# Kernel tuning notes

Measured on AMD Instinct MI355X. Metric: run time of the kernel, lower is better.

The kernel has to match this reference:

```python
import jax, jax.numpy as jnp
import numpy as np

EMBED_DIM = 1024
NUM_HEADS = 16
HEAD_DIM = EMBED_DIM // NUM_HEADS
BATCH = 2
SEQ = 2048


def setup_inputs() -> dict:
    key = jax.random.key(0)
    ks = jax.random.split(key, 10)
    s = 1.0 / np.sqrt(EMBED_DIM)
    inp = {
        "query": jax.random.normal(ks[0], (BATCH, SEQ, EMBED_DIM), jnp.float32),
        # Linear weights stored as [in, out] (y = x @ W + b)
        "wq": jax.random.normal(ks[1], (EMBED_DIM, EMBED_DIM), jnp.float32) * s,
        "bq": jnp.zeros((EMBED_DIM,), jnp.float32),
        "wk": jax.random.normal(ks[2], (EMBED_DIM, EMBED_DIM), jnp.float32) * s,
        "bk": jnp.zeros((EMBED_DIM,), jnp.float32),
        "wv": jax.random.normal(ks[3], (EMBED_DIM, EMBED_DIM), jnp.float32) * s,
        "bv": jnp.zeros((EMBED_DIM,), jnp.float32),
        "wo": jax.random.normal(ks[4], (EMBED_DIM, EMBED_DIM), jnp.float32) * s,
        "bo": jnp.zeros((EMBED_DIM,), jnp.float32),
        "temperature": jnp.float32(HEAD_DIM),  # learnable temperature, init = head_dim
    }
    return inp


def reference(query, wq, bq, wk, bk, wv, bv, wo, bo, temperature):
    B, S, E = query.shape
    # self-attention: key = value = query
    Q = (query @ wq + bq).reshape(B, S, NUM_HEADS, HEAD_DIM).transpose(0, 2, 1, 3)
    K = (query @ wk + bk).reshape(B, S, NUM_HEADS, HEAD_DIM).transpose(0, 2, 1, 3)
    V = (query @ wv + bv).reshape(B, S, NUM_HEADS, HEAD_DIM).transpose(0, 2, 1, 3)
    # squared Euclidean distances: ||q||^2 + ||k||^2 - 2<q,k>
    q_sq = jnp.sum(Q * Q, axis=-1, keepdims=True)          # (B,H,Sq,1)
    k_sq = jnp.sum(K * K, axis=-1, keepdims=True)          # (B,H,Sk,1)
    qk = jnp.einsum("bhqd,bhkd->bhqk", Q, K)
    d_sq = jnp.maximum(q_sq + jnp.swapaxes(k_sq, -2, -1) - 2.0 * qk, 0.0)
    attn = jax.nn.softmax(-d_sq / temperature, axis=-1)    # (B,H,Sq,Sk)
    out = jnp.einsum("bhqk,bhkd->bhqd", attn, V)
    out = out.transpose(0, 2, 1, 3).reshape(B, S, E)
    return out @ wo + bo
```

## Files before the change

### kernel.cpp

```cpp
#include <hip/hip_runtime.h>
#include <stdint.h>
#include <stddef.h>


#define LOG2E 1.44269504088896f

typedef __attribute__((ext_vector_type(8))) short bf16x8;
typedef __attribute__((ext_vector_type(4))) float f32x4;
typedef __attribute__((ext_vector_type(4))) unsigned short u16x4;

__device__ __forceinline__ unsigned short f2b(float f) {
  union { float f; unsigned int u; } x; x.f = f;
  unsigned int u = x.u;
  u += 0x7fffu + ((u >> 16) & 1u);
  return (unsigned short)(u >> 16);
}
__device__ __forceinline__ float b2f(unsigned short s) {
  union { unsigned int u; float f; } x; x.u = ((unsigned int)s) << 16;
  return x.f;
}
__device__ __forceinline__ unsigned int fbits(float f) {
  union { float f; unsigned int u; } x; x.f = f; return x.u;
}

#define GLD_LDS(g, l) __builtin_amdgcn_global_load_lds( \
    (const __attribute__((address_space(1))) void*)(g), \
    (__attribute__((address_space(3))) void*)(l), 16, 0, 0)

__global__ void prep_kernel(const float* __restrict__ X,
                            const float* __restrict__ wq, const float* __restrict__ wk,
                            const float* __restrict__ wv, const float* __restrict__ wo,
                            unsigned short* __restrict__ Xb,
                            unsigned short* __restrict__ WTqkv, unsigned short* __restrict__ WTo) {
  int z = blockIdx.z;
  if (z == 4) {
    size_t base = ((size_t)(blockIdx.y * 16 + blockIdx.x)) * 16384;
    #pragma unroll
    for (int j = 0; j < 16; ++j) {
      size_t i = base + (size_t)(j * 256 + threadIdx.x) * 4;
      f32x4 v = *(const f32x4*)&X[i];
      u16x4 o;
      #pragma unroll
      for (int k = 0; k < 4; ++k) o[k] = f2b(v[k]);
      *(u16x4*)&Xb[i] = o;
    }
    return;
  }
  __shared__ float tile[64][65];
  const float* src = (z == 0) ? wq : (z == 1) ? wk : (z == 2) ? wv : wo;
  unsigned short* dst = (z < 3) ? (WTqkv + (size_t)z * 1024 * 1024) : WTo;
  int k0 = blockIdx.y * 64, n0 = blockIdx.x * 64;
  int rr = threadIdx.x >> 6, cc = threadIdx.x & 63;
  #pragma unroll
  for (int p = 0; p < 16; ++p) {
    int row = p * 4 + rr;
    tile[row][cc] = src[(size_t)(k0 + row) * 1024 + n0 + cc];
  }
  __syncthreads();
  #pragma unroll
  for (int p = 0; p < 16; ++p) {
    int row = p * 4 + rr;
    dst[(size_t)(n0 + row) * 1024 + k0 + cc] = f2b(tile[cc][row]);
  }
}

__global__ __launch_bounds__(256, 3) void gemm_qkv_kernel(
    const unsigned short* __restrict__ X, const unsigned short* __restrict__ WT,
    const float* __restrict__ bq, const float* __restrict__ bk, const float* __restrict__ bv,
    const float* __restrict__ temp,
    unsigned short* __restrict__ Qb, unsigned short* __restrict__ Kb,
    unsigned short* __restrict__ VTo, float* __restrict__ ks2) {
  __shared__ __align__(16) unsigned short smem[16896];
  unsigned short* As = smem;
  unsigned short* Bs = smem + 8192;
  const int t = threadIdx.x, w = t >> 6, lane = t & 63;
  const int r = lane & 15, q4 = lane >> 4;
  const int m0 = blockIdx.y * 128, n0 = blockIdx.x * 128;
  const int wr = (w >> 1) * 64, wc = (w & 1) * 64;
  const unsigned short* Xg = X + (size_t)m0 * 1024;
  const unsigned short* Wg = WT + (size_t)n0 * 1024;
  f32x4 acc[4][4] = {};
  for (int k0 = 0; k0 < 1024; k0 += 64) {
    #pragma unroll
    for (int g = 0; g < 4; ++g) {
      int slot = g * 256 + t;
      int kh = slot >> 9, row = (slot >> 2) & 127, ko = (slot & 3) * 8;
      GLD_LDS(Xg + (size_t)row * 1024 + k0 + kh * 32 + ko, &As[(g * 256 + w * 64) * 8]);
      GLD_LDS(Wg + (size_t)row * 1024 + k0 + kh * 32 + ko, &Bs[(g * 256 + w * 64) * 8]);
    }
    __syncthreads();
    #pragma unroll
    for (int kh = 0; kh < 2; ++kh) {
      bf16x8 af[4], bfr[4];
      #pragma unroll
      for (int mf = 0; mf < 4; ++mf)
        af[mf] = *(const bf16x8*)&As[kh * 4096 + (wr + mf * 16 + r) * 32 + q4 * 8];
      #pragma unroll
      for (int nf = 0; nf < 4; ++nf)
        bfr[nf] = *(const bf16x8*)&Bs[kh * 4096 + (wc + nf * 16 + r) * 32 + q4 * 8];
      #pragma unroll
      for (int mf = 0; mf < 4; ++mf)
        #pragma unroll
        for (int nf = 0; nf < 4; ++nf)
          acc[mf][nf] = __builtin_amdgcn_mfma_f32_16x16x32_bf16(af[mf], bfr[nf], acc[mf][nf], 0, 0, 0);
    }
    __syncthreads();
  }
  const int nblk = n0 >> 10;
  if (nblk == 0) {
    const int nc0 = n0 & 1023;
    #pragma unroll
    for (int nf = 0; nf < 4; ++nf) {
      int n = nc0 + wc + nf * 16 + r;
      float bb = bq[n];
      #pragma unroll
      for (int mf = 0; mf < 4; ++mf) {
        int m = m0 + wr + mf * 16 + q4 * 4;
        f32x4 v = acc[mf][nf];
        #pragma unroll
        for (int i = 0; i < 4; ++i)
          Qb[(size_t)(m + i) * 1024 + n] = f2b(v[i] + bb);
      }
    }
  } else if (nblk == 1) {
    const float sc = LOG2E / temp[0];
    const int nc0 = n0 & 1023;
    float s2a[4][4] = {};
    #pragma unroll
    for (int nf = 0; nf < 4; ++nf) {
      int n = nc0 + wc + nf * 16 + r;
      float bb = bk[n];
      #pragma unroll
      for (int mf = 0; mf < 4; ++mf) {
        int m = m0 + wr + mf * 16 + q4 * 4;
        f32x4 v = acc[mf][nf];
        #pragma unroll
        for (int i = 0; i < 4; ++i) {
          unsigned short os = f2b(v[i] + bb);
          Kb[(size_t)(m + i) * 1024 + n] = os;
          float xb = b2f(os);
          s2a[mf][i] += xb * xb;
        }
      }
    }
    #pragma unroll
    for (int mf = 0; mf < 4; ++mf)
      #pragma unroll
      for (int i = 0; i < 4; ++i) {
        float v = s2a[mf][i];
        v += __shfl_xor(v, 1, 64);
        v += __shfl_xor(v, 2, 64);
        v += __shfl_xor(v, 4, 64);
        v += __shfl_xor(v, 8, 64);
        s2a[mf][i] = v * sc;
      }
    if (r == 0) {
      int hh = (nc0 + wc) >> 6;
      #pragma unroll
      for (int mf = 0; mf < 4; ++mf) {
        int m = m0 + wr + mf * 16 + q4 * 4;
        int bb2 = m >> 11, ss = m & 2047;
        #pragma unroll
        for (int i = 0; i < 4; ++i)
          ks2[(size_t)(bb2 * 16 + hh) * 2048 + ss + i] = s2a[mf][i];
      }
    }
  } else {
    unsigned short* Vt = smem;
    const int c0 = n0 - 2048;
    const int head = w & 1;
    #pragma unroll
    for (int nf = 0; nf < 4; ++nf) {
      int c = c0 + wc + nf * 16 + r;
      float bb = bv[c];
      int d = c & 63;
      #pragma unroll
      for (int mf = 0; mf < 4; ++mf) {
        int mloc = wr + mf * 16 + q4 * 4;
        int G = mloc >> 6;
        int k6 = mloc & 63;
        int pos = (k6 >> 5) * 32 + ((k6 & 15) >> 2) * 8 + ((k6 >> 4) & 1) * 4;
        f32x4 v = acc[mf][nf];
        u16x4 pk;
        #pragma unroll
        for (int i = 0; i < 4; ++i) pk[i] = f2b(v[i] + bb);
        *(u16x4*)&Vt[(head * 64 + d) * 132 + G * 64 + pos] = pk;
      }
    }
    __syncthreads();
    int row = t >> 1, ch = t & 1;
    int hd = row >> 6, dd = row & 63;
    int hglob = (c0 >> 6) + hd;
    int bb2 = m0 >> 11, s0 = m0 & 2047;
    unsigned short* dst = &VTo[((size_t)((bb2 * 16 + hglob) * 64 + dd)) * 2048 + s0 + ch * 64];
    const unsigned short* srcL = &Vt[(hd * 64 + dd) * 132 + ch * 64];
    #pragma unroll
    for (int k2 = 0; k2 < 16; ++k2)
      *(u16x4*)&dst[k2 * 4] = *(const u16x4*)&srcL[k2 * 4];
  }
}

__global__ __launch_bounds__(256, 2) void flash_kernel(
    const unsigned short* __restrict__ Qb, const unsigned short* __restrict__ Kb,
    const unsigned short* __restrict__ VT, const float* __restrict__ ks2,
    const float* __restrict__ temp, unsigned short* __restrict__ AO) {
  __shared__ __align__(16) unsigned short Ks[3][64 * 64];
  __shared__ __align__(16) unsigned short Vs[3][64 * 64];
  __shared__ __align__(16) float KQs[2048];
  const int t = threadIdx.x, w = t >> 6, lane = t & 63;
  const int r = lane & 15, q4 = lane >> 4;
  const int wgid = blockIdx.x + 16 * blockIdx.y;
  const int xcd = wgid & 7, s = wgid >> 3;
  const int bh = xcd + 8 * (s & 3);
  const int b = bh >> 4, h = bh & 15;
  const int q0 = (s >> 2) * 128;
  const float cc = 2.0f * LOG2E / temp[0];

  bf16x8 qf[2][2];
  #pragma unroll
  for (int qg = 0; qg < 2; ++qg) {
    int sq = q0 + w * 32 + qg * 16 + r;
    const unsigned short* qp = Qb + (size_t)(b * 2048 + sq) * 1024 + h * 64;
    #pragma unroll
    for (int ks = 0; ks < 2; ++ks) qf[qg][ks] = *(const bf16x8*)(qp + ks * 32 + q4 * 8);
  }

  f32x4 accO[2][4] = {};
  f32x4 lsum[2] = {};
  bf16x8 ones;
  #pragma unroll
  for (int j = 0; j < 8; ++j) ones[j] = (short)0x3F80;

  const unsigned short* Kg = Kb + ((size_t)b * 2048) * 1024 + h * 64;
  const unsigned short* Vg = VT + ((size_t)bh * 64) * 2048;
  const float* kqb = ks2 + bh * 2048;

  const unsigned short* kp0 = Kg + (size_t)(t >> 2) * 1024 + (t & 3) * 8;
  const unsigned short* kp1 = kp0 + 32;
  int dd0 = t >> 3;
  const unsigned short* vp0 = Vg + (size_t)dd0 * 2048 + ((t & 7) ^ (dd0 & 7)) * 8;
  const unsigned short* vp1 = vp0 + (size_t)32 * 2048;

  GLD_LDS(kqb + t * 4, &KQs[t * 4]);
  GLD_LDS(kqb + 1024 + t * 4, &KQs[1024 + t * 4]);
  GLD_LDS(kp0, &Ks[0][t * 8]);
  GLD_LDS(kp1, &Ks[0][(256 + t) * 8]);
  GLD_LDS(vp0, &Vs[0][t * 8]);
  GLD_LDS(vp1, &Vs[0][(256 + t) * 8]);
  kp0 += 65536; kp1 += 65536; vp0 += 64; vp1 += 64;
  GLD_LDS(kp0, &Ks[1][t * 8]);
  GLD_LDS(kp1, &Ks[1][(256 + t) * 8]);
  GLD_LDS(vp0, &Vs[1][t * 8]);
  GLD_LDS(vp1, &Vs[1][(256 + t) * 8]);
  kp0 += 65536; kp1 += 65536; vp0 += 64; vp1 += 64;

  const unsigned short* k_cur = &Ks[0][0];
  const unsigned short* k_nxt = &Ks[1][0];
  const unsigned short* k_fre = &Ks[2][0];
  const unsigned short* v_cur = &Vs[0][0];
  const unsigned short* v_nxt = &Vs[1][0];
  const unsigned short* v_fre = &Vs[2][0];

  #pragma unroll 2
  for (int c = 0; c < 32; ++c) {
    __builtin_amdgcn_s_barrier();
    if (c < 30) {
      GLD_LDS(kp0, (unsigned short*)k_fre + t * 8);
      GLD_LDS(kp1, (unsigned short*)k_fre + (256 + t) * 8);
      GLD_LDS(vp0, (unsigned short*)v_fre + t * 8);
      GLD_LDS(vp1, (unsigned short*)v_fre + (256 + t) * 8);
      kp0 += 65536; kp1 += 65536; vp0 += 64; vp1 += 64;
      asm volatile("s_waitcnt vmcnt(8)" ::: "memory");
    } else if (c == 30) {
      asm volatile("s_waitcnt vmcnt(4)" ::: "memory");
    } else {
      asm volatile("s_waitcnt vmcnt(0)" ::: "memory");
    }
    __builtin_amdgcn_s_barrier();
    __builtin_amdgcn_sched_barrier(0);

    f32x4 kq[4];
    #pragma unroll
    for (int kfm = 0; kfm < 4; ++kfm)
      kq[kfm] = *(const f32x4*)&KQs[c * 64 + kfm * 16 + q4 * 4];

    f32x4 accST[2][4] = {};
    __builtin_amdgcn_s_setprio(1);
    #pragma unroll
    for (int ks = 0; ks < 2; ++ks) {
      #pragma unroll
      for (int kfm = 0; kfm < 4; ++kfm) {
        bf16x8 ka = *(const bf16x8*)&k_cur[(ks * 64 + kfm * 16 + r) * 32 + q4 * 8];
        accST[0][kfm] = __builtin_amdgcn_mfma_f32_16x16x32_bf16(ka, qf[0][ks], accST[0][kfm], 0, 0, 0);
        accST[1][kfm] = __builtin_amdgcn_mfma_f32_16x16x32_bf16(ka, qf[1][ks], accST[1][kfm], 0, 0, 0);
      }
    }
    __builtin_amdgcn_s_setprio(0);

    bf16x8 pf[2][2];
    #pragma unroll
    for (int qg = 0; qg < 2; ++qg) {
      #pragma unroll
      for (int cb = 0; cb < 2; ++cb) {
        unsigned int dw[4];
        #pragma unroll
        for (int half = 0; half < 2; ++half) {
          int kfm = cb * 2 + half;
          float pp[4];
          #pragma unroll
          for (int i = 0; i < 4; ++i) {
            float u = __builtin_fmaf(cc, accST[qg][kfm][i], -kq[kfm][i]);
            pp[i] = __builtin_amdgcn_exp2f(u);
          }
          dw[half * 2 + 0] = (fbits(pp[0]) >> 16) | (fbits(pp[1]) & 0xFFFF0000u);
          dw[half * 2 + 1] = (fbits(pp[2]) >> 16) | (fbits(pp[3]) & 0xFFFF0000u);
        }
        union { unsigned int d[4]; bf16x8 v; } cv;
        cv.d[0] = dw[0]; cv.d[1] = dw[1]; cv.d[2] = dw[2]; cv.d[3] = dw[3];
        pf[qg][cb] = cv.v;
      }
    }

    __builtin_amdgcn_s_setprio(1);
    #pragma unroll
    for (int cb = 0; cb < 2; ++cb) {
      lsum[0] = __builtin_amdgcn_mfma_f32_16x16x32_bf16(pf[0][cb], ones, lsum[0], 0, 0, 0);
      lsum[1] = __builtin_amdgcn_mfma_f32_16x16x32_bf16(pf[1][cb], ones, lsum[1], 0, 0, 0);
      #pragma unroll
      for (int df = 0; df < 4; ++df) {
        int dloc = df * 16 + r;
        int un = dloc * 8 + ((cb * 4 + q4) ^ (dloc & 7));
        bf16x8 vb = *(const bf16x8*)&v_cur[un * 8];
        accO[0][df] = __builtin_amdgcn_mfma_f32_16x16x32_bf16(pf[0][cb], vb, accO[0][df], 0, 0, 0);
        accO[1][df] = __builtin_amdgcn_mfma_f32_16x16x32_bf16(pf[1][cb], vb, accO[1][df], 0, 0, 0);
      }
    }
    __builtin_amdgcn_s_setprio(0);

    const unsigned short* tk = k_cur; k_cur = k_nxt; k_nxt = k_fre; k_fre = tk;
    const unsigned short* tv = v_cur; v_cur = v_nxt; v_nxt = v_fre; v_fre = tv;
  }
  #pragma unroll
  for (int qg = 0; qg < 2; ++qg) {
    float inv[4];
    #pragma unroll
    for (int i = 0; i < 4; ++i) inv[i] = 1.0f / lsum[qg][i];
    #pragma unroll
    for (int df = 0; df < 4; ++df) {
      int d = df * 16 + r;
      #pragma unroll
      for (int i = 0; i < 4; ++i) {
        int sq = q0 + w * 32 + qg * 16 + q4 * 4 + i;
        AO[(size_t)(b * 2048 + sq) * 1024 + h * 64 + d] = f2b(accO[qg][df][i] * inv[i]);
      }
    }
  }
}

__global__ __launch_bounds__(256, 2) void gemm_out_kernel(
    const unsigned short* __restrict__ A, const unsigned short* __restrict__ WT,
    const float* __restrict__ bo, float* __restrict__ Out) {
  __shared__ __align__(16) unsigned short As[2 * 128 * 32];
  __shared__ __align__(16) unsigned short Bs[2 * 64 * 32];
  const int t = threadIdx.x, w = t >> 6, lane = t & 63;
  const int r = lane & 15, q4 = lane >> 4;
  const int m0 = blockIdx.y * 128, n0 = blockIdx.x * 64;
  const int wr = (w >> 1) * 64, wc = (w & 1) * 32;
  const unsigned short* Ag = A + (size_t)m0 * 1024;
  const unsigned short* Wg = WT + (size_t)n0 * 1024;
  f32x4 acc[4][2] = {};
  for (int k0 = 0; k0 < 1024; k0 += 64) {
    #pragma unroll
    for (int g = 0; g < 4; ++g) {
      int slot = g * 256 + t;
      int kh = slot >> 9, row = (slot >> 2) & 127, ko = (slot & 3) * 8;
      GLD_LDS(Ag + (size_t)row * 1024 + k0 + kh * 32 + ko, &As[(g * 256 + w * 64) * 8]);
    }
    #pragma unroll
    for (int g = 0; g < 2; ++g) {
      int slot = g * 256 + t;
      int kh = slot >> 8, row = (slot >> 2) & 63, ko = (slot & 3) * 8;
      GLD_LDS(Wg + (size_t)row * 1024 + k0 + kh * 32 + ko, &Bs[(g * 256 + w * 64) * 8]);
    }
    __syncthreads();
    #pragma unroll
    for (int kh = 0; kh < 2; ++kh) {
      bf16x8 af[4], bfr[2];
      #pragma unroll
      for (int mf = 0; mf < 4; ++mf)
        af[mf] = *(const bf16x8*)&As[kh * 4096 + (wr + mf * 16 + r) * 32 + q4 * 8];
      #pragma unroll
      for (int nf = 0; nf < 2; ++nf)
        bfr[nf] = *(const bf16x8*)&Bs[kh * 2048 + (wc + nf * 16 + r) * 32 + q4 * 8];
      #pragma unroll
      for (int mf = 0; mf < 4; ++mf)
        #pragma unroll
        for (int nf = 0; nf < 2; ++nf)
          acc[mf][nf] = __builtin_amdgcn_mfma_f32_16x16x32_bf16(af[mf], bfr[nf], acc[mf][nf], 0, 0, 0);
    }
    __syncthreads();
  }
  #pragma unroll
  for (int nf = 0; nf < 2; ++nf) {
    int n = n0 + wc + nf * 16 + r;
    float bb = bo[n];
    #pragma unroll
    for (int mf = 0; mf < 4; ++mf) {
      int m = m0 + wr + mf * 16 + q4 * 4;
      f32x4 v = acc[mf][nf];
      #pragma unroll
      for (int i = 0; i < 4; ++i)
        Out[(size_t)(m + i) * 1024 + n] = v[i] + bb;
    }
  }
}

extern "C" void kernel_launch(void* const* d_in, const int* in_sizes, int n_in,
                              void* d_out, int out_size, void* d_ws, size_t ws_size,
                              hipStream_t stream) {
  const float* X    = (const float*)d_in[0];
  const float* wq   = (const float*)d_in[1];
  const float* bq   = (const float*)d_in[2];
  const float* wk   = (const float*)d_in[3];
  const float* bk   = (const float*)d_in[4];
  const float* wv   = (const float*)d_in[5];
  const float* bv   = (const float*)d_in[6];
  const float* wo   = (const float*)d_in[7];
  const float* bo   = (const float*)d_in[8];
  const float* temp = (const float*)d_in[9];
  float* Out = (float*)d_out;

  char* ws = (char*)d_ws;
  unsigned short* Xb    = (unsigned short*)ws; ws += (size_t)4096 * 1024 * 2;
  unsigned short* WTqkv = (unsigned short*)ws; ws += (size_t)3072 * 1024 * 2;
  unsigned short* WTo   = (unsigned short*)ws; ws += (size_t)1024 * 1024 * 2;
  unsigned short* Qb    = (unsigned short*)ws; ws += (size_t)4096 * 1024 * 2;
  unsigned short* Kb    = (unsigned short*)ws; ws += (size_t)4096 * 1024 * 2;
  unsigned short* VT    = (unsigned short*)ws; ws += (size_t)4096 * 1024 * 2;
  float* ks2 = (float*)ws; ws += (size_t)65536 * 4;
  unsigned short* AO = Xb;

  prep_kernel<<<dim3(16, 16, 5), 256, 0, stream>>>(X, wq, wk, wv, wo, Xb, WTqkv, WTo);
  gemm_qkv_kernel<<<dim3(24, 32), 256, 0, stream>>>(Xb, WTqkv, bq, bk, bv, temp, Qb, Kb, VT, ks2);
  flash_kernel<<<dim3(16, 32), 256, 0, stream>>>(Qb, Kb, VT, ks2, temp, AO);
  gemm_out_kernel<<<dim3(16, 32), 256, 0, stream>>>(AO, WTo, bo, Out);
}
```

Baseline: 188.7 us.

## Software-pipeline QK^T one chunk ahead of softmax and PV in flash kernel

```diff
diff --git a/kernel.cpp b/kernel.cpp
--- a/kernel.cpp
+++ b/kernel.cpp
@@ -204,7 +204,7 @@
     const unsigned short* __restrict__ Qb, const unsigned short* __restrict__ Kb,
     const unsigned short* __restrict__ VT, const float* __restrict__ ks2,
     const float* __restrict__ temp, unsigned short* __restrict__ AO) {
-  __shared__ __align__(16) unsigned short Ks[3][64 * 64];
+  __shared__ __align__(16) unsigned short Ks[2][64 * 64];
   __shared__ __align__(16) unsigned short Vs[3][64 * 64];
   __shared__ __align__(16) float KQs[2048];
   const int t = threadIdx.x, w = t >> 6, lane = t & 63;
@@ -254,104 +254,131 @@
   GLD_LDS(vp1, &Vs[1][(256 + t) * 8]);
   kp0 += 65536; kp1 += 65536; vp0 += 64; vp1 += 64;
 
-  const unsigned short* k_cur = &Ks[0][0];
-  const unsigned short* k_nxt = &Ks[1][0];
-  const unsigned short* k_fre = &Ks[2][0];
   const unsigned short* v_cur = &Vs[0][0];
   const unsigned short* v_nxt = &Vs[1][0];
   const unsigned short* v_fre = &Vs[2][0];
 
-  #pragma unroll 2
-  for (int c = 0; c < 32; ++c) {
-    __builtin_amdgcn_s_barrier();
-    if (c < 30) {
-      GLD_LDS(kp0, (unsigned short*)k_fre + t * 8);
-      GLD_LDS(kp1, (unsigned short*)k_fre + (256 + t) * 8);
-      GLD_LDS(vp0, (unsigned short*)v_fre + t * 8);
-      GLD_LDS(vp1, (unsigned short*)v_fre + (256 + t) * 8);
-      kp0 += 65536; kp1 += 65536; vp0 += 64; vp1 += 64;
-      asm volatile("s_waitcnt vmcnt(8)" ::: "memory");
-    } else if (c == 30) {
-      asm volatile("s_waitcnt vmcnt(4)" ::: "memory");
-    } else {
-      asm volatile("s_waitcnt vmcnt(0)" ::: "memory");
-    }
-    __builtin_amdgcn_s_barrier();
-    __builtin_amdgcn_sched_barrier(0);
-
-    f32x4 kq[4];
-    #pragma unroll
-    for (int kfm = 0; kfm < 4; ++kfm)
-      kq[kfm] = *(const f32x4*)&KQs[c * 64 + kfm * 16 + q4 * 4];
-
-    f32x4 accST[2][4] = {};
+  asm volatile("s_waitcnt vmcnt(4)" ::: "memory");
+  __builtin_amdgcn_s_barrier();
+  __builtin_amdgcn_sched_barrier(0);
+
+  f32x4 stA[2][4], stB[2][4];
+  {
+    const f32x4 zz = {};
     __builtin_amdgcn_s_setprio(1);
     #pragma unroll
     for (int ks = 0; ks < 2; ++ks) {
       #pragma unroll
       for (int kfm = 0; kfm < 4; ++kfm) {
-        bf16x8 ka = *(const bf16x8*)&k_cur[(ks * 64 + kfm * 16 + r) * 32 + q4 * 8];
-        accST[0][kfm] = __builtin_amdgcn_mfma_f32_16x16x32_bf16(ka, qf[0][ks], accST[0][kfm], 0, 0, 0);
-        accST[1][kfm] = __builtin_amdgcn_mfma_f32_16x16x32_bf16(ka, qf[1][ks], accST[1][kfm], 0, 0, 0);
+        bf16x8 ka = *(const bf16x8*)&Ks[0][(ks * 64 + kfm * 16 + r) * 32 + q4 * 8];
+        stA[0][kfm] = __builtin_amdgcn_mfma_f32_16x16x32_bf16(ka, qf[0][ks], ks ? stA[0][kfm] : zz, 0, 0, 0);
+        stA[1][kfm] = __builtin_amdgcn_mfma_f32_16x16x32_bf16(ka, qf[1][ks], ks ? stA[1][kfm] : zz, 0, 0, 0);
       }
     }
     __builtin_amdgcn_s_setprio(0);
-
-    bf16x8 pf[2][2];
+  }
+
+#define CHUNK_BODY(C, STC, STN)                                               \
+  {                                                                           \
+    const int c_ = (C);                                                       \
+    __builtin_amdgcn_s_barrier();                                             \
+    if (c_ < 30) {                                                            \
+      unsigned short* kdst = &Ks[(C) & 1][0];                                 \
+      GLD_LDS(kp0, kdst + t * 8);                                             \
+      GLD_LDS(kp1, kdst + (256 + t) * 8);                                     \
+      GLD_LDS(vp0, (unsigned short*)v_fre + t * 8);                           \
+      GLD_LDS(vp1, (unsigned short*)v_fre + (256 + t) * 8);                   \
+      kp0 += 65536; kp1 += 65536; vp0 += 64; vp1 += 64;                       \
+      asm volatile("s_waitcnt vmcnt(4)" ::: "memory");                        \
+    } else {                                                                  \
+      asm volatile("s_waitcnt vmcnt(0)" ::: "memory");                        \
+    }                                                                         \
+    __builtin_amdgcn_s_barrier();                                             \
+    __builtin_amdgcn_sched_barrier(0);                                        \
+                 \
+    if (c_ < 31) {                                                            \
+      const unsigned short* krd = &Ks[((C) + 1) & 1][0];                      \
+      const f32x4 zz = {};                                                    \
+      __builtin_amdgcn_s_setprio(1);                                          \
+      _Pragma("unroll")                                                       \
+      for (int ks = 0; ks < 2; ++ks) {                                        \
+        _Pragma("unroll")                                                     \
+        for (int kfm = 0; kfm < 4; ++kfm) {                                   \
+          bf16x8 ka = *(const bf16x8*)&krd[(ks * 64 + kfm * 16 + r) * 32 + q4 * 8]; \
+          STN[0][kfm] = __builtin_amdgcn_mfma_f32_16x16x32_bf16(ka, qf[0][ks], ks ? STN[0][kfm] : zz, 0, 0, 0); \
+          STN[1][kfm] = __builtin_amdgcn_mfma_f32_16x16x32_bf16(ka, qf[1][ks], ks ? STN[1][kfm] : zz, 0, 0, 0); \
+        }                                                                     \
+      }                                                                       \
+      __builtin_amdgcn_s_setprio(0);                                          \
+    }                                                                         \
+                                \
+    f32x4 kq[4];                                                              \
+    _Pragma("unroll")                                                         \
+    for (int kfm = 0; kfm < 4; ++kfm)                                         \
+      kq[kfm] = *(const f32x4*)&KQs[c_ * 64 + kfm * 16 + q4 * 4];             \
+    bf16x8 pf[2][2];                                                          \
+    _Pragma("unroll")                                                         \
+    for (int qg = 0; qg < 2; ++qg) {                                          \
+      _Pragma("unroll")                                                       \
+      for (int cb = 0; cb < 2; ++cb) {                                        \
+        unsigned int dw[4];                                                   \
+        _Pragma("unroll")                                                     \
+        for (int half = 0; half < 2; ++half) {                                \
+          int kfm = cb * 2 + half;                                            \
+          float pp[4];                                                        \
+          _Pragma("unroll")                                                   \
+          for (int i = 0; i < 4; ++i) {                                       \
+            float u = __builtin_fmaf(cc, STC[qg][kfm][i], -kq[kfm][i]);       \
+            pp[i] = __builtin_amdgcn_exp2f(u);                                \
+          }                                                                   \
+          dw[half * 2 + 0] = (fbits(pp[0]) >> 16) | (fbits(pp[1]) & 0xFFFF0000u); \
+          dw[half * 2 + 1] = (fbits(pp[2]) >> 16) | (fbits(pp[3]) & 0xFFFF0000u); \
+        }                                                                     \
+        union { unsigned int d[4]; bf16x8 v; } cv;                            \
+        cv.d[0] = dw[0]; cv.d[1] = dw[1]; cv.d[2] = dw[2]; cv.d[3] = dw[3];   \
+        pf[qg][cb] = cv.v;                                                    \
+      }                                                                       \
+    }                                                                         \
+        \
+    __builtin_amdgcn_s_setprio(1);                                            \
+    _Pragma("unroll")                                                         \
+    for (int cb = 0; cb < 2; ++cb) {                                          \
+      lsum[0] = __builtin_amdgcn_mfma_f32_16x16x32_bf16(pf[0][cb], ones, lsum[0], 0, 0, 0); \
+      lsum[1] = __builtin_amdgcn_mfma_f32_16x16x32_bf16(pf[1][cb], ones, lsum[1], 0, 0, 0); \
+      _Pragma("unroll")                                                       \
+      for (int df = 0; df < 4; ++df) {                                        \
+        int dloc = df * 16 + r;                                               \
+        int un = dloc * 8 + ((cb * 4 + q4) ^ (dloc & 7));                     \
+        bf16x8 vb = *(const bf16x8*)&v_cur[un * 8];                           \
+        accO[0][df] = __builtin_amdgcn_mfma_f32_16x16x32_bf16(pf[0][cb], vb, accO[0][df], 0, 0, 0); \
+        accO[1][df] = __builtin_amdgcn_mfma_f32_16x16x32_bf16(pf[1][cb], vb, accO[1][df], 0, 0, 0); \
+      }                                                                       \
+    }                                                                         \
+    __builtin_amdgcn_s_setprio(0);                                            \
+                                                        \
+    const unsigned short* tv = v_cur; v_cur = v_nxt; v_nxt = v_fre; v_fre = tv; \
+  }
+
+  for (int c2 = 0; c2 < 16; ++c2) {
+    CHUNK_BODY(2 * c2, stA, stB)
+    CHUNK_BODY(2 * c2 + 1, stB, stA)
+  }
+#undef CHUNK_BODY
+
+  {
     #pragma unroll
     for (int qg = 0; qg < 2; ++qg) {
-      #pragma unroll
-      for (int cb = 0; cb < 2; ++cb) {
-        unsigned int dw[4];
-        #pragma unroll
-        for (int half = 0; half < 2; ++half) {
-          int kfm = cb * 2 + half;
-          float pp[4];
-          #pragma unroll
-          for (int i = 0; i < 4; ++i) {
-            float u = __builtin_fmaf(cc, accST[qg][kfm][i], -kq[kfm][i]);
-            pp[i] = __builtin_amdgcn_exp2f(u);
-          }
-          dw[half * 2 + 0] = (fbits(pp[0]) >> 16) | (fbits(pp[1]) & 0xFFFF0000u);
-          dw[half * 2 + 1] = (fbits(pp[2]) >> 16) | (fbits(pp[3]) & 0xFFFF0000u);
+      float inv[4];
+      #pragma unroll
+      for (int i = 0; i < 4; ++i) inv[i] = 1.0f / lsum[qg][i];
+      #pragma unroll
+      for (int df = 0; df < 4; ++df) {
+        int d = df * 16 + r;
+        #pragma unroll
+        for (int i = 0; i < 4; ++i) {
+          int sq = q0 + w * 32 + qg * 16 + q4 * 4 + i;
+          AO[(size_t)(b * 2048 + sq) * 1024 + h * 64 + d] = f2b(accO[qg][df][i] * inv[i]);
         }
-        union { unsigned int d[4]; bf16x8 v; } cv;
-        cv.d[0] = dw[0]; cv.d[1] = dw[1]; cv.d[2] = dw[2]; cv.d[3] = dw[3];
-        pf[qg][cb] = cv.v;
-      }
-    }
-
-    __builtin_amdgcn_s_setprio(1);
-    #pragma unroll
-    for (int cb = 0; cb < 2; ++cb) {
-      lsum[0] = __builtin_amdgcn_mfma_f32_16x16x32_bf16(pf[0][cb], ones, lsum[0], 0, 0, 0);
-      lsum[1] = __builtin_amdgcn_mfma_f32_16x16x32_bf16(pf[1][cb], ones, lsum[1], 0, 0, 0);
-      #pragma unroll
-      for (int df = 0; df < 4; ++df) {
-        int dloc = df * 16 + r;
-        int un = dloc * 8 + ((cb * 4 + q4) ^ (dloc & 7));
-        bf16x8 vb = *(const bf16x8*)&v_cur[un * 8];
-        accO[0][df] = __builtin_amdgcn_mfma_f32_16x16x32_bf16(pf[0][cb], vb, accO[0][df], 0, 0, 0);
-        accO[1][df] = __builtin_amdgcn_mfma_f32_16x16x32_bf16(pf[1][cb], vb, accO[1][df], 0, 0, 0);
-      }
-    }
-    __builtin_amdgcn_s_setprio(0);
-
-    const unsigned short* tk = k_cur; k_cur = k_nxt; k_nxt = k_fre; k_fre = tk;
-    const unsigned short* tv = v_cur; v_cur = v_nxt; v_nxt = v_fre; v_fre = tv;
-  }
-  #pragma unroll
-  for (int qg = 0; qg < 2; ++qg) {
-    float inv[4];
-    #pragma unroll
-    for (int i = 0; i < 4; ++i) inv[i] = 1.0f / lsum[qg][i];
-    #pragma unroll
-    for (int df = 0; df < 4; ++df) {
-      int d = df * 16 + r;
-      #pragma unroll
-      for (int i = 0; i < 4; ++i) {
-        int sq = q0 + w * 32 + qg * 16 + q4 * 4 + i;
-        AO[(size_t)(b * 2048 + sq) * 1024 + h * 64 + d] = f2b(accO[qg][df][i] * inv[i]);
       }
     }
   }
```

New measurement: 189.1 us. Within noise of the previous version (+0.2%).
